# Performance work log

Measured on AMD Instinct MI355X. Metric: run time of the kernel, lower is better.

Reference implementation:

```python
import jax, jax.numpy as jnp
import numpy as np

E = 128          # embedding_dim
H = 128          # decoder_hidden_dim
N = 200000       # number of candidate nodes


def setup_inputs() -> dict:
    key = jax.random.key(0)
    k0, k1, k2, k3, k4, k5 = jax.random.split(key, 6)
    return {
        "current_node_emb": jax.random.normal(k0, (1, E), jnp.float32),
        "context_emb": jax.random.normal(k1, (1, E), jnp.float32),
        "candidate_node_embs": jax.random.normal(k2, (N, E), jnp.float32),
        "Wq": jax.random.normal(k3, (H, 2 * E), jnp.float32) * 0.05,  # nn.Linear(2E->H, bias=False) weight
        "Wk": jax.random.normal(k4, (H, E), jnp.float32) * 0.05,      # nn.Linear(E->H, bias=False) weight
        "mask": jax.random.randint(k5, (1, N), 0, 2, jnp.int32),
    }


def reference(current_node_emb, context_emb, candidate_node_embs, Wq, Wk, mask):
    # combined_input = cat([current, context], dim=1) -> [1, 2E]
    combined = jnp.concatenate([current_node_emb, context_emb], axis=1)
    query = combined @ Wq.T                      # [1, H]
    keys = candidate_node_embs @ Wk.T            # [N, H]
    attn_scores = query @ keys.T                 # [1, N]
    masked = jnp.where(mask == 0, -jnp.inf, attn_scores)
    probs = jax.nn.softmax(masked, axis=1)       # [1, N]

    n = probs.shape[1]
    k = min(50, max(1, int(0.5 * n)))            # static Python int -> jit-friendly
    top_probs, _ = jax.lax.top_k(probs, k)       # [1, k]
    threshold = top_probs[:, -1:]                # [1, 1]
    top_mask = probs >= threshold
    filtered = probs * top_mask
    filtered = filtered / (jnp.sum(filtered, axis=1, keepdims=True) + 1e-10)

    log_probs_all = jnp.log(filtered + 1e-10)    # [1, N]
    # Categorical(filtered): true-zero probability outside top-k
    logits = jnp.where(filtered > 0, jnp.log(filtered), -jnp.inf)
    action_idx = jax.random.categorical(jax.random.key(42), logits, axis=1)  # [1]
    log_prob_action = jnp.take_along_axis(logits, action_idx[:, None], axis=1)[:, 0]  # [1]
    return (log_probs_all, log_prob_action, action_idx)
```

## Files before the change

### kernel.cpp

```cpp
#include <hip/hip_runtime.h>
#include <math.h>


#define SLOT 4096
#define MAXB 64
#define C2CAP 2048
#define NEG_INF (-__builtin_inff())

__device__ __forceinline__ unsigned int f2ord(float f){
  unsigned int b = __float_as_uint(f);
  return (b & 0x80000000u) ? ~b : (b | 0x80000000u);
}
__device__ __forceinline__ unsigned int rotl32(unsigned int x, int d){
  return (x << d) | (x >> (32 - d));
}

__device__ float gumbel_from_idx(unsigned int idx){
  unsigned int x0 = 0u, x1 = idx;
  const unsigned int ks0 = 0u, ks1 = 42u;
  const unsigned int ks2 = 0u ^ 42u ^ 0x1BD11BDAu;
  x0 += ks0; x1 += ks1;
#define TF_RND(r) { x0 += x1; x1 = rotl32(x1, (r)); x1 ^= x0; }
  TF_RND(13) TF_RND(15) TF_RND(26) TF_RND(6)
  x0 += ks1; x1 += ks2 + 1u;
  TF_RND(17) TF_RND(29) TF_RND(16) TF_RND(24)
  x0 += ks2; x1 += ks0 + 2u;
  TF_RND(13) TF_RND(15) TF_RND(26) TF_RND(6)
  x0 += ks0; x1 += ks1 + 3u;
  TF_RND(17) TF_RND(29) TF_RND(16) TF_RND(24)
  x0 += ks1; x1 += ks2 + 4u;
  TF_RND(13) TF_RND(15) TF_RND(26) TF_RND(6)
  x0 += ks2; x1 += ks0 + 5u;
#undef TF_RND
  unsigned int bits = x0 ^ x1;
  unsigned int fb = (bits >> 9) | 0x3f800000u;
  float f = __uint_as_float(fb) - 1.0f;
  float u = (f < 1.17549435e-38f) ? 1.17549435e-38f : f;
  return -logf(-logf(u));
}

__device__ void hist_select(unsigned int* lh, unsigned int* suf, int* csel_sh,
                            unsigned int* u_lo_sh, int ktop, int t){
  if (t < 256){
    unsigned int csum = 0;
    #pragma unroll
    for (int k = 0; k < 8; ++k) csum += lh[t * 8 + k];
    suf[t] = csum;
  }
  __syncthreads();
  for (int d = 1; d < 256; d <<= 1){
    unsigned int add = 0u;
    if (t < 256 && t + d < 256) add = suf[t + d];
    __syncthreads();
    if (t < 256) suf[t] += add;
    __syncthreads();
  }
  if (t < 256){
    unsigned int st = suf[t];
    unsigned int sn = (t < 255) ? suf[t + 1] : 0u;
    if (st >= (unsigned)ktop && sn < (unsigned)ktop) *csel_sh = t;
  }
  __syncthreads();
  if (t == 0){
    int b_sel = 0;
    int c = *csel_sh;
    if (c >= 0){
      unsigned int cum = (c < 255) ? suf[c + 1] : 0u;
      for (int bi = 8 * c + 7; bi >= 8 * c; --bi){
        cum += lh[bi];
        if (cum >= (unsigned)ktop){ b_sel = bi; break; }
      }
    }
    *u_lo_sh = ((unsigned int)b_sel) << 21;
  }
  __syncthreads();
}

__global__ __launch_bounds__(256) void k_prep(const float* __restrict__ cur,
    const float* __restrict__ ctx, const float* __restrict__ Wq,
    const float* __restrict__ Wk, float* __restrict__ v,
    unsigned int* __restrict__ hist, unsigned int* __restrict__ scal_u){
  __shared__ float q[128];
  __shared__ float vpart[256];
  int t = threadIdx.x;
  int lane = t & 63, wave = t >> 6;
  int hl = lane & 31, hi = lane >> 5;
  for (int k = t; k < 2048; k += 256) hist[k] = 0u;
  if (t < 16) scal_u[t] = 0u;
  float4 cb0 = ((const float4*)cur)[hl];
  float4 cb1 = ((const float4*)ctx)[hl];
  const float4* Wq4 = (const float4*)Wq;
  #pragma unroll 4
  for (int i = 0; i < 16; ++i){
    int row = wave * 32 + 2 * i + hi;
    float4 w0 = Wq4[row * 64 + hl];
    float4 w1 = Wq4[row * 64 + 32 + hl];
    float d = fmaf(w0.x, cb0.x, fmaf(w0.y, cb0.y, fmaf(w0.z, cb0.z, w0.w * cb0.w)));
    d = fmaf(w1.x, cb1.x, fmaf(w1.y, cb1.y, fmaf(w1.z, cb1.z, fmaf(w1.w, cb1.w, d))));
    d += __shfl_xor(d, 1, 64);
    d += __shfl_xor(d, 2, 64);
    d += __shfl_xor(d, 4, 64);
    d += __shfl_xor(d, 8, 64);
    d += __shfl_xor(d, 16, 64);
    if (hl == 0) q[row] = d;
  }
  __syncthreads();
  int col = t & 127, half = t >> 7;
  const float* wkp = Wk + half * 64 * 128 + col;
  const float* qp  = q + half * 64;
  float acc = 0.f;
  #pragma unroll 8
  for (int h = 0; h < 64; ++h) acc = fmaf(qp[h], wkp[h * 128], acc);
  vpart[t] = acc;
  __syncthreads();
  if (t < 128) v[t] = vpart[t] + vpart[t + 128];
}

__global__ __launch_bounds__(256) void k_score(const float* __restrict__ cand,
    const int* __restrict__ mask, const float* __restrict__ v,
    float* __restrict__ scores, float* __restrict__ out, int N){
  const float NLOG = logf(1e-10f);
  int t = threadIdx.x;
  int lane = t & 63, wave = t >> 6;
  int hi = lane >> 5, hl = lane & 31;
  float4 v4 = ((const float4*)v)[hl];
  const float4* cp = (const float4*)cand;
  int base = (blockIdx.x * 4 + wave) * 16;
  float4 c[8];
  #pragma unroll
  for (int k = 0; k < 8; ++k){
    int r = base + 2 * k + hi;
    r = (r < N) ? r : (N - 1);
    c[k] = cp[(size_t)r * 32 + hl];
  }
  float p[8];
  #pragma unroll
  for (int k = 0; k < 8; ++k)
    p[k] = fmaf(c[k].x, v4.x, fmaf(c[k].y, v4.y, fmaf(c[k].z, v4.z, c[k].w * v4.w)));
  #pragma unroll
  for (int k = 0; k < 8; ++k){
    p[k] += __shfl_xor(p[k], 1, 64);
    p[k] += __shfl_xor(p[k], 2, 64);
    p[k] += __shfl_xor(p[k], 4, 64);
    p[k] += __shfl_xor(p[k], 8, 64);
    p[k] += __shfl_xor(p[k], 16, 64);
  }
  float sv = p[0];
  #pragma unroll
  for (int k = 1; k < 8; ++k) sv = (hl == k) ? p[k] : sv;
  if (hl < 8){
    int r = base + 2 * hl + hi;
    if (r < N) scores[r] = mask[r] ? sv : NEG_INF;
  }
  if (t < 16){
    int o4 = blockIdx.x * 16 + t;
    if (o4 * 4 + 3 < N){
      ((float4*)out)[o4] = make_float4(NLOG, NLOG, NLOG, NLOG);
    } else {
      #pragma unroll
      for (int e = 0; e < 4; ++e){ int i = o4 * 4 + e; if (i < N) out[i] = NLOG; }
    }
  }
}

__global__ __launch_bounds__(1024) void k_tail(const float* __restrict__ scores,
    unsigned int* __restrict__ scal_u, unsigned int* __restrict__ hist,
    float* __restrict__ zpart, unsigned int* __restrict__ cnt,
    unsigned int* __restrict__ buf_idx, float* __restrict__ buf_s,
    float* __restrict__ out, int N, int ktop, int nb){
  __shared__ unsigned int lh[2048];
  __shared__ unsigned int suf[256];
  __shared__ float s2[C2CAP];
  __shared__ unsigned int i2[C2CAP];
  __shared__ unsigned int cnt_l[MAXB], offs[MAXB];
  __shared__ float wred[16];
  __shared__ float rv[16], rl[16];
  __shared__ unsigned int ri[16];
  __shared__ float Z_sh, thr_sh, lnD_sh;
  __shared__ unsigned int u_lo_sh;
  __shared__ int csel_sh, pos_sh, C_sh, last_sh;
  int t = threadIdx.x, b = blockIdx.x;
  int lane = t & 63, wave = t >> 6;
  for (int k = t; k < 2048; k += 1024) lh[k] = 0u;
  if (t == 0){ pos_sh = 0; csel_sh = -1; }
  __syncthreads();
  int base = b * 4096;
  int i0 = base + 4 * t;
  float4 s4 = make_float4(NEG_INF, NEG_INF, NEG_INF, NEG_INF);
  if (i0 + 3 < N) s4 = ((const float4*)scores)[(base >> 2) + t];
  else {
    if (i0     < N) s4.x = scores[i0];
    if (i0 + 1 < N) s4.y = scores[i0 + 1];
    if (i0 + 2 < N) s4.z = scores[i0 + 2];
  }
  float ez = 0.f;
#define HVISIT(s_) { float sx = (s_); if (sx > NEG_INF){ \
    atomicAdd(&lh[f2ord(sx) >> 21], 1u); ez += expf(sx); } }
  HVISIT(s4.x) HVISIT(s4.y) HVISIT(s4.z) HVISIT(s4.w)
#undef HVISIT
  #pragma unroll
  for (int off = 32; off; off >>= 1) ez += __shfl_xor(ez, off, 64);
  if (lane == 0) wred[wave] = ez;
  __syncthreads();
  hist_select(lh, suf, &csel_sh, &u_lo_sh, ktop, t);
  unsigned int u_lo = u_lo_sh;
#define GVISIT(s_, i_) { float sx = (s_); \
    if (sx > NEG_INF && f2ord(sx) >= u_lo && (i_) < N){ \
      int p = atomicAdd(&pos_sh, 1); \
      buf_s[(size_t)b * SLOT + p] = sx; \
      buf_idx[(size_t)b * SLOT + p] = (unsigned int)(i_); } }
  GVISIT(s4.x, i0) GVISIT(s4.y, i0 + 1) GVISIT(s4.z, i0 + 2) GVISIT(s4.w, i0 + 3)
#undef GVISIT
  for (int k = t; k < 2048; k += 1024){
    unsigned int cc = lh[k];
    if (cc) atomicAdd(&hist[k], cc);
  }
  __syncthreads();
  if (t == 0){
    cnt[b] = (unsigned int)pos_sh;
    float z = 0.f;
    for (int w = 0; w < 16; ++w) z += wred[w];
    zpart[b] = z;
    __threadfence();
    unsigned int old = atomicAdd(&scal_u[8], 1u);
    last_sh = (old == (unsigned)(nb - 1));
  }
  __syncthreads();
  if (!last_sh) return;
  __threadfence();
  if (t < nb) cnt_l[t] = cnt[t];
  for (int k = t; k < 2048; k += 1024) lh[k] = hist[k];
  {
    float z = 0.f;
    if (t < 64){
      z = (t < nb) ? zpart[t] : 0.f;
      #pragma unroll
      for (int off = 32; off; off >>= 1) z += __shfl_xor(z, off, 64);
    }
    if (t == 0){ Z_sh = z; thr_sh = NEG_INF; pos_sh = 0; csel_sh = -1; }
  }
  __syncthreads();
  if (t == 0){
    unsigned int acc = 0;
    for (int b2 = 0; b2 < nb; ++b2){ offs[b2] = acc; acc += cnt_l[b2]; }
    C_sh = (int)acc;
  }
  __syncthreads();
  hist_select(lh, suf, &csel_sh, &u_lo_sh, ktop, t);
  unsigned int u_lo2 = u_lo_sh;
  int C = C_sh;
  for (int p = t; p < C; p += 1024){
    int lo = 0, hi2 = nb - 1;
    while (lo < hi2){
      int mid = (lo + hi2 + 1) >> 1;
      if (offs[mid] <= (unsigned)p) lo = mid; else hi2 = mid - 1;
    }
    unsigned int j = (unsigned)p - offs[lo];
    float sx = buf_s[(size_t)lo * SLOT + j];
    if (sx > NEG_INF && f2ord(sx) >= u_lo2){
      int q = atomicAdd(&pos_sh, 1);
      if (q < C2CAP){ s2[q] = sx; i2[q] = buf_idx[(size_t)lo * SLOT + j]; }
    }
  }
  __syncthreads();
  int C2 = (pos_sh > C2CAP) ? C2CAP : pos_sh;
  if (C2 > ktop){
    for (int j = t; j < C2; j += 1024){
      float sj = s2[j];
      int g = 0, e = 0;
      for (int k2 = 0; k2 < C2; ++k2){
        float sk = s2[k2];
        g += (sk > sj);
        e += (sk == sj);
      }
      if (g < ktop && g + e >= ktop) thr_sh = sj;
    }
  }
  __syncthreads();
  float s_thr = thr_sh;
  float part = 0.f;
  for (int j = t; j < C2; j += 1024){
    float sj = s2[j];
    if (sj >= s_thr) part += expf(sj);
  }
  #pragma unroll
  for (int off = 32; off; off >>= 1) part += __shfl_xor(part, off, 64);
  if (lane == 0) wred[wave] = part;
  __syncthreads();
  if (t == 0){
    float T = 0.f;
    for (int w = 0; w < 16; ++w) T += wred[w];
    lnD_sh = logf(T + 1e-10f * Z_sh);
  }
  __syncthreads();
  float lnD = lnD_sh;
  for (int j = t; j < C2; j += 1024){
    float sj = s2[j];
    if (sj >= s_thr) out[i2[j]] = logf(expf(sj - lnD) + 1e-10f);
  }
  float bestv = NEG_INF, bestlogit = NEG_INF;
  unsigned int bestidx = 0xFFFFFFFFu;
  for (int j = t; j < C2; j += 1024){
    float sj = s2[j];
    if (sj >= s_thr){
      unsigned int idx = i2[j];
      float logit = sj - lnD;
      float val = logit + gumbel_from_idx(idx);
      if (val > bestv || (val == bestv && idx < bestidx)){
        bestv = val; bestlogit = logit; bestidx = idx;
      }
    }
  }
  #pragma unroll
  for (int off = 32; off; off >>= 1){
    float ov = __shfl_xor(bestv, off, 64);
    float ol = __shfl_xor(bestlogit, off, 64);
    unsigned int oi = (unsigned int)__shfl_xor((int)bestidx, off, 64);
    if (ov > bestv || (ov == bestv && oi < bestidx)){
      bestv = ov; bestlogit = ol; bestidx = oi;
    }
  }
  if (lane == 0){ rv[wave] = bestv; rl[wave] = bestlogit; ri[wave] = bestidx; }
  __syncthreads();
  if (t == 0){
    for (int w = 1; w < 16; ++w){
      if (rv[w] > rv[0] || (rv[w] == rv[0] && ri[w] < ri[0])){
        rv[0] = rv[w]; rl[0] = rl[w]; ri[0] = ri[w];
      }
    }
    out[N] = rl[0];
    out[N + 1] = (float)ri[0];
  }
}

extern "C" void kernel_launch(void* const* d_in, const int* in_sizes, int n_in,
                              void* d_out, int out_size, void* d_ws, size_t ws_size,
                              hipStream_t stream){
  const float* cur  = (const float*)d_in[0];
  const float* ctx  = (const float*)d_in[1];
  const float* cand = (const float*)d_in[2];
  const float* Wq   = (const float*)d_in[3];
  const float* Wk   = (const float*)d_in[4];
  const int*   mask = (const int*)d_in[5];
  int N = in_sizes[5];
  float* out = (float*)d_out;

  char* ws = (char*)d_ws;
  unsigned int* scal_u  = (unsigned int*)ws;
  float*        v       = (float*)(ws + 512);
  float*        zpart   = (float*)(ws + 1024);
  unsigned int* cnt     = (unsigned int*)(ws + 1536);
  unsigned int* hist    = (unsigned int*)(ws + 4096);
  float*        scores  = (float*)(ws + 16384);
  char*         bufbase = ws + 16384 + (((size_t)N * 4 + 255) & ~255ull);
  float*        buf_s   = (float*)bufbase;
  unsigned int* buf_idx = (unsigned int*)(bufbase + (size_t)MAXB * SLOT * 4);

  int ktop = N / 2; if (ktop < 1) ktop = 1; if (ktop > 50) ktop = 50;
  int g_score = (N + 63) / 64;
  int nb = (N + 4095) / 4096;
  if (nb > MAXB) nb = MAXB;

  k_prep<<<1, 256, 0, stream>>>(cur, ctx, Wq, Wk, v, hist, scal_u);
  k_score<<<g_score, 256, 0, stream>>>(cand, mask, v, scores, out, N);
  k_tail<<<nb, 1024, 0, stream>>>(scores, scal_u, hist, zpart, cnt,
                                  buf_idx, buf_s, out, N, ktop, nb);
}
```

Baseline: 206.2 us.

## Fuse query projection into score kernel and skip loading masked candidate rows

Removes the separate single-block prep kernel. Every score block now recomputes the projected query vector from Wq and Wk in shared memory, and the workspace zeroing is spread across a few blocks. The mask is loaded first, and candidate rows whose mask is zero are not fetched, which cuts global memory traffic for the large embedding matrix. In exchange, every block repeats the Wq/Wk reads and the reductions, which adds L2 traffic and latency at the start of each block.

```diff
diff --git a/kernel.cpp b/kernel.cpp
--- a/kernel.cpp
+++ b/kernel.cpp
@@ -76,62 +76,72 @@
   __syncthreads();
 }
 
-__global__ __launch_bounds__(256) void k_prep(const float* __restrict__ cur,
+__global__ __launch_bounds__(256) void k_score(const float* __restrict__ cur,
     const float* __restrict__ ctx, const float* __restrict__ Wq,
-    const float* __restrict__ Wk, float* __restrict__ v,
-    unsigned int* __restrict__ hist, unsigned int* __restrict__ scal_u){
+    const float* __restrict__ Wk, const float* __restrict__ cand,
+    const int* __restrict__ mask, unsigned int* __restrict__ hist,
+    unsigned int* __restrict__ scal_u, float* __restrict__ scores,
+    float* __restrict__ out, int N){
+  const float NLOG = logf(1e-10f);
   __shared__ float q[128];
   __shared__ float vpart[256];
-  int t = threadIdx.x;
-  int lane = t & 63, wave = t >> 6;
-  int hl = lane & 31, hi = lane >> 5;
-  for (int k = t; k < 2048; k += 256) hist[k] = 0u;
-  if (t < 16) scal_u[t] = 0u;
-  float4 cb0 = ((const float4*)cur)[hl];
-  float4 cb1 = ((const float4*)ctx)[hl];
-  const float4* Wq4 = (const float4*)Wq;
-  #pragma unroll 4
-  for (int i = 0; i < 16; ++i){
-    int row = wave * 32 + 2 * i + hi;
-    float4 w0 = Wq4[row * 64 + hl];
-    float4 w1 = Wq4[row * 64 + 32 + hl];
-    float d = fmaf(w0.x, cb0.x, fmaf(w0.y, cb0.y, fmaf(w0.z, cb0.z, w0.w * cb0.w)));
-    d = fmaf(w1.x, cb1.x, fmaf(w1.y, cb1.y, fmaf(w1.z, cb1.z, fmaf(w1.w, cb1.w, d))));
-    d += __shfl_xor(d, 1, 64);
-    d += __shfl_xor(d, 2, 64);
-    d += __shfl_xor(d, 4, 64);
-    d += __shfl_xor(d, 8, 64);
-    d += __shfl_xor(d, 16, 64);
-    if (hl == 0) q[row] = d;
-  }
-  __syncthreads();
-  int col = t & 127, half = t >> 7;
-  const float* wkp = Wk + half * 64 * 128 + col;
-  const float* qp  = q + half * 64;
-  float acc = 0.f;
-  #pragma unroll 8
-  for (int h = 0; h < 64; ++h) acc = fmaf(qp[h], wkp[h * 128], acc);
-  vpart[t] = acc;
-  __syncthreads();
-  if (t < 128) v[t] = vpart[t] + vpart[t + 128];
-}
-
-__global__ __launch_bounds__(256) void k_score(const float* __restrict__ cand,
-    const int* __restrict__ mask, const float* __restrict__ v,
-    float* __restrict__ scores, float* __restrict__ out, int N){
-  const float NLOG = logf(1e-10f);
+  __shared__ float vsh[128];
   int t = threadIdx.x;
   int lane = t & 63, wave = t >> 6;
   int hi = lane >> 5, hl = lane & 31;
-  float4 v4 = ((const float4*)v)[hl];
-  const float4* cp = (const float4*)cand;
   int base = (blockIdx.x * 4 + wave) * 16;
-  float4 c[8];
+  int m[8];
   #pragma unroll
   for (int k = 0; k < 8; ++k){
     int r = base + 2 * k + hi;
     r = (r < N) ? r : (N - 1);
-    c[k] = cp[(size_t)r * 32 + hl];
+    m[k] = mask[r];
+  }
+  if (gridDim.x >= 16){
+    if (blockIdx.x >= 1 && blockIdx.x <= 8) hist[(blockIdx.x - 1) * 256 + t] = 0u;
+    if (blockIdx.x == 9 && t < 16) scal_u[t] = 0u;
+  } else if (blockIdx.x == 0){
+    for (int k = t; k < 2048; k += 256) hist[k] = 0u;
+    if (t < 16) scal_u[t] = 0u;
+  }
+  {
+    float4 cb0 = ((const float4*)cur)[hl];
+    float4 cb1 = ((const float4*)ctx)[hl];
+    const float4* Wq4 = (const float4*)Wq;
+    #pragma unroll 4
+    for (int i = 0; i < 16; ++i){
+      int row = wave * 32 + 2 * i + hi;
+      float4 w0 = Wq4[row * 64 + hl];
+      float4 w1 = Wq4[row * 64 + 32 + hl];
+      float d = fmaf(w0.x, cb0.x, fmaf(w0.y, cb0.y, fmaf(w0.z, cb0.z, w0.w * cb0.w)));
+      d = fmaf(w1.x, cb1.x, fmaf(w1.y, cb1.y, fmaf(w1.z, cb1.z, fmaf(w1.w, cb1.w, d))));
+      d += __shfl_xor(d, 1, 64);
+      d += __shfl_xor(d, 2, 64);
+      d += __shfl_xor(d, 4, 64);
+      d += __shfl_xor(d, 8, 64);
+      d += __shfl_xor(d, 16, 64);
+      if (hl == 0) q[row] = d;
+    }
+    __syncthreads();
+    int col = t & 127, half = t >> 7;
+    const float* wkp = Wk + half * 64 * 128 + col;
+    const float* qp  = q + half * 64;
+    float acc = 0.f;
+    #pragma unroll 8
+    for (int h = 0; h < 64; ++h) acc = fmaf(qp[h], wkp[h * 128], acc);
+    vpart[t] = acc;
+    __syncthreads();
+    if (t < 128) vsh[t] = vpart[t] + vpart[t + 128];
+    __syncthreads();
+  }
+  float4 v4 = ((const float4*)vsh)[hl];
+  float4 c[8];
+  #pragma unroll
+  for (int k = 0; k < 8; ++k){
+    int r = base + 2 * k + hi;
+    r = (r < N) ? r : (N - 1);
+    c[k] = make_float4(0.f, 0.f, 0.f, 0.f);
+    if (m[k]) c[k] = ((const float4*)cand)[(size_t)r * 32 + hl];
   }
   float p[8];
   #pragma unroll
@@ -347,7 +357,6 @@
 
   char* ws = (char*)d_ws;
   unsigned int* scal_u  = (unsigned int*)ws;
-  float*        v       = (float*)(ws + 512);
   float*        zpart   = (float*)(ws + 1024);
   unsigned int* cnt     = (unsigned int*)(ws + 1536);
   unsigned int* hist    = (unsigned int*)(ws + 4096);
@@ -361,8 +370,8 @@
   int nb = (N + 4095) / 4096;
   if (nb > MAXB) nb = MAXB;
 
-  k_prep<<<1, 256, 0, stream>>>(cur, ctx, Wq, Wk, v, hist, scal_u);
-  k_score<<<g_score, 256, 0, stream>>>(cand, mask, v, scores, out, N);
+  k_score<<<g_score, 256, 0, stream>>>(cur, ctx, Wq, Wk, cand, mask,
+                                       hist, scal_u, scores, out, N);
   k_tail<<<nb, 1024, 0, stream>>>(scores, scal_u, hist, zpart, cnt,
                                   buf_idx, buf_s, out, N, ktop, nb);
 }
```

After: 205.8 us. No clear change (-0.2%).
